# Optimization experiments

Measured on AMD Instinct MI355X. Metric: run time of the kernel, lower is better.

## Reference

```python
import jax, jax.numpy as jnp
import numpy as np

BATCH = 2048
VOCAB = 50257
TOPK = 512


def setup_inputs() -> dict:
    key = jax.random.key(0)
    k1, k2 = jax.random.split(key)
    features = jax.random.normal(k1, (BATCH, VOCAB), dtype=jnp.float32)
    labels = jax.random.randint(k2, (BATCH,), 0, VOCAB, dtype=jnp.int64 if jax.config.jax_enable_x64 else jnp.int32)
    return {"features": features, "labels": labels, "k": TOPK}


def reference(features, labels, k):
    # features: [B, V], labels: [B], k: python int (top-k count)
    # Original per-sample loop computes: -log(exp(feat_label) / sum(exp(topk(row))))
    # Vectorized: mean over batch of (log(sum(exp(topk_vals))) - feat_label).
    feat_label = jnp.take_along_axis(features, labels[:, None].astype(jnp.int32), axis=1)[:, 0]  # [B]
    topk_vals, _ = jax.lax.top_k(features, k)  # [B, k]
    lse = jnp.log(jnp.sum(jnp.exp(topk_vals), axis=-1))  # [B] (matches original non-stabilized math)
    return jnp.mean(lse - feat_label)
```

## Files before the change

### kernel.cpp

```cpp
#include <hip/hip_runtime.h>
#include <cstdint>
#include <cstddef>

#define BATCH 2048
#define VOCAB 50257
#define TOPK  512
#define CAND_MAX 4096
#define BLOCK 256

typedef float vfloat4 __attribute__((ext_vector_type(4)));

__device__ __forceinline__ unsigned fkey(float f) {
    unsigned u = __float_as_uint(f);
    return (u & 0x80000000u) ? ~u : (u | 0x80000000u);
}
__device__ __forceinline__ float unfkey(unsigned k) {
    unsigned u = (k & 0x80000000u) ? (k & 0x7FFFFFFFu) : ~k;
    return __uint_as_float(u);
}

__global__ __launch_bounds__(BLOCK) void topk_ce_kernel(
    const float* __restrict__ feats,
    const int*   __restrict__ labels,
    float*       __restrict__ out)
{
    __shared__ float    cand[CAND_MAX];
    __shared__ int      s_cnt;
    __shared__ unsigned s_hist[256];
    __shared__ unsigned s_sfx[256];
    __shared__ int      s_dig, s_above;
    __shared__ float    s_psum[BLOCK / 64];
    __shared__ float    s_pcnt[BLOCK / 64];

    const int row = blockIdx.x;
    const int tid = threadIdx.x;
    const float* rp = feats + (size_t)row * VOCAB;

    uintptr_t a = (uintptr_t)rp;
    int head = ((int)((16u - (a & 15u)) & 15u)) >> 2;
    if (head > VOCAB) head = VOCAB;
    const int nvec = (VOCAB - head) >> 2;
    const int tailstart = head + nvec * 4;
    const vfloat4* vp = (const vfloat4*)(rp + head);
    const int nfull = nvec / (BLOCK * 4);
    const int restart = nfull * BLOCK * 4;

    float thresh = 2.0f;
    float blo = 0.0f, bhi = 0.0f;
    bool  has_lo = false, has_hi = false;
    float step = 1.0f;
    int   n_cand = 0;

#define APPEND1(x) do { if ((x) > thresh) { int p_ = atomicAdd(&s_cnt, 1); \
                        if (p_ < CAND_MAX) cand[p_] = (x); } } while (0)
#define APPEND4(v) do { APPEND1((v).x); APPEND1((v).y); APPEND1((v).z); APPEND1((v).w); } while (0)

    for (int attempt = 0; attempt < 40; ++attempt) {
        if (tid == 0) s_cnt = 0;
        __syncthreads();

        for (int i = tid; i < head; i += BLOCK) {
            float v = rp[i];
            APPEND1(v);
        }
        for (int it = 0; it < nfull; ++it) {
            const int base = it * (BLOCK * 4) + tid;
            vfloat4 v0 = __builtin_nontemporal_load(&vp[base]);
            vfloat4 v1 = __builtin_nontemporal_load(&vp[base + BLOCK]);
            vfloat4 v2 = __builtin_nontemporal_load(&vp[base + 2 * BLOCK]);
            vfloat4 v3 = __builtin_nontemporal_load(&vp[base + 3 * BLOCK]);
            APPEND4(v0); APPEND4(v1); APPEND4(v2); APPEND4(v3);
        }
        for (int i = restart + tid; i < nvec; i += BLOCK) {
            vfloat4 v = __builtin_nontemporal_load(&vp[i]);
            APPEND4(v);
        }
        for (int i = tailstart + tid; i < VOCAB; i += BLOCK) {
            float v = rp[i];
            APPEND1(v);
        }
        __syncthreads();
        n_cand = s_cnt;
        if (n_cand >= TOPK && n_cand <= CAND_MAX) break;
        if (n_cand < TOPK) { bhi = thresh; has_hi = true; }
        else               { blo = thresh; has_lo = true; }
        if (has_lo && has_hi)      thresh = 0.5f * (blo + bhi);
        else if (has_lo)          { thresh = blo + step; step *= 2.0f; }
        else                      { thresh = bhi - step; step *= 2.0f; }
        __syncthreads();
    }

    const int m  = (n_cand < CAND_MAX) ? n_cand : CAND_MAX;
    const int kk = (TOPK < m) ? TOPK : m;
    if (m == 0) return;

    unsigned pref = 0, maskhi = 0;
    int remain = kk;
    const int m_pad = ((m + BLOCK - 1) / BLOCK) * BLOCK;

    for (int sh = 24; sh >= 0; sh -= 8) {
        s_hist[tid] = 0;
        __syncthreads();

        for (int i = tid; i < m_pad; i += BLOCK) {
            bool valid = (i < m);
            unsigned key = valid ? fkey(cand[i]) : 0u;
            bool match = valid && ((key & maskhi) == pref);
            unsigned dig = (key >> sh) & 255u;
            unsigned long long mm = __ballot(match);
            if (mm) {
                int leader = __ffsll((unsigned long long)mm) - 1;
                unsigned ldig = __shfl(dig, leader);
                unsigned long long same = __ballot(match && (dig == ldig));
                if (same == mm) {
                    if ((tid & 63) == leader)
                        atomicAdd(&s_hist[ldig], (unsigned)__popcll(mm));
                } else if (match) {
                    atomicAdd(&s_hist[dig], 1u);
                }
            }
        }
        __syncthreads();

        s_sfx[tid] = s_hist[tid];
        __syncthreads();
        for (int off = 1; off < 256; off <<= 1) {
            unsigned add = (tid + off < 256) ? s_sfx[tid + off] : 0u;
            __syncthreads();
            s_sfx[tid] += add;
            __syncthreads();
        }
        unsigned my  = s_sfx[tid];
        unsigned nxt = (tid < 255) ? s_sfx[tid + 1] : 0u;
        if ((int)my >= remain && (tid == 255 || (int)nxt < remain)) {
            s_dig = tid;
            s_above = (int)nxt;
        }
        __syncthreads();
        remain -= s_above;
        pref   |= ((unsigned)s_dig) << sh;
        maskhi |= (0xFFu << sh);
        __syncthreads();
    }

    const float tval = unfkey(pref);

    float psum = 0.0f, pcnt = 0.0f;
    for (int i = tid; i < m; i += BLOCK) {
        float v = cand[i];
        if (fkey(v) > pref) { psum += expf(v); pcnt += 1.0f; }
    }
    for (int off = 32; off > 0; off >>= 1) {
        psum += __shfl_down(psum, off);
        pcnt += __shfl_down(pcnt, off);
    }
    const int lane = tid & 63, wid = tid >> 6;
    if (lane == 0) { s_psum[wid] = psum; s_pcnt[wid] = pcnt; }
    __syncthreads();
    if (tid == 0) {
        float sum = 0.0f, cnt = 0.0f;
        for (int w = 0; w < BLOCK / 64; ++w) { sum += s_psum[w]; cnt += s_pcnt[w]; }
        sum += ((float)kk - cnt) * expf(tval);
        float fl = rp[labels[row]];
        float loss = logf(sum) - fl;
        atomicAdd(out, loss * (1.0f / (float)BATCH));
    }
}

extern "C" void kernel_launch(void* const* d_in, const int* in_sizes, int n_in,
                              void* d_out, int out_size, void* d_ws, size_t ws_size,
                              hipStream_t stream) {
    const float* feats  = (const float*)d_in[0];
    const int*   labels = (const int*)d_in[1];
    float* out = (float*)d_out;
    (void)in_sizes; (void)n_in; (void)out_size; (void)d_ws; (void)ws_size;

    (void)hipMemsetAsync(out, 0, sizeof(float), stream);
    topk_ce_kernel<<<BATCH, BLOCK, 0, stream>>>(feats, labels, out);
}
```

Measured before the change: 525.2 us.

## Replace shared atomic candidate append with per-thread LDS buckets and prefix compaction

```diff
diff --git a/kernel.cpp b/kernel.cpp
--- a/kernel.cpp
+++ b/kernel.cpp
@@ -5,8 +5,10 @@
 #define BATCH 2048
 #define VOCAB 50257
 #define TOPK  512
-#define CAND_MAX 4096
 #define BLOCK 256
+#define SLOTS 16
+#define STRIDE 17
+#define CAND_MAX (BLOCK * SLOTS)
 
 typedef float vfloat4 __attribute__((ext_vector_type(4)));
 
@@ -24,17 +26,17 @@
     const int*   __restrict__ labels,
     float*       __restrict__ out)
 {
-    __shared__ float    cand[CAND_MAX];
-    __shared__ int      s_cnt;
+    __shared__ float    buck[BLOCK * STRIDE];
+    __shared__ unsigned s_pfx[BLOCK];
     __shared__ unsigned s_hist[256];
-    __shared__ unsigned s_sfx[256];
-    __shared__ int      s_dig, s_above;
-    __shared__ float    s_psum[BLOCK / 64];
-    __shared__ float    s_pcnt[BLOCK / 64];
+    __shared__ int      s_dig, s_above, s_ovf;
+    __shared__ float    s_red0[BLOCK / 64];
+    __shared__ float    s_red1[BLOCK / 64];
 
     const int row = blockIdx.x;
     const int tid = threadIdx.x;
     const float* rp = feats + (size_t)row * VOCAB;
+    const int bbase = tid * STRIDE;
 
     uintptr_t a = (uintptr_t)rp;
     int head = ((int)((16u - (a & 15u)) & 15u)) >> 2;
@@ -49,50 +51,71 @@
     float blo = 0.0f, bhi = 0.0f;
     bool  has_lo = false, has_hi = false;
     float step = 1.0f;
-    int   n_cand = 0;
-
-#define APPEND1(x) do { if ((x) > thresh) { int p_ = atomicAdd(&s_cnt, 1); \
-                        if (p_ < CAND_MAX) cand[p_] = (x); } } while (0)
-#define APPEND4(v) do { APPEND1((v).x); APPEND1((v).y); APPEND1((v).z); APPEND1((v).w); } while (0)
+    int   cnt = 0;
+    unsigned total = 0;
+
+#define PUT1(x) do { float xv_ = (x); \
+                     int idx_ = (cnt < SLOTS) ? cnt : (SLOTS - 1); \
+                     buck[bbase + idx_] = xv_; \
+                     cnt += (xv_ > thresh) ? 1 : 0; } while (0)
+#define PUT4(v) do { PUT1((v).x); PUT1((v).y); PUT1((v).z); PUT1((v).w); } while (0)
 
     for (int attempt = 0; attempt < 40; ++attempt) {
-        if (tid == 0) s_cnt = 0;
-        __syncthreads();
-
-        for (int i = tid; i < head; i += BLOCK) {
-            float v = rp[i];
-            APPEND1(v);
-        }
+        if (tid == 0) s_ovf = 0;
+        cnt = 0;
+        __syncthreads();
+
+        for (int i = tid; i < head; i += BLOCK) PUT1(rp[i]);
         for (int it = 0; it < nfull; ++it) {
             const int base = it * (BLOCK * 4) + tid;
             vfloat4 v0 = __builtin_nontemporal_load(&vp[base]);
             vfloat4 v1 = __builtin_nontemporal_load(&vp[base + BLOCK]);
             vfloat4 v2 = __builtin_nontemporal_load(&vp[base + 2 * BLOCK]);
             vfloat4 v3 = __builtin_nontemporal_load(&vp[base + 3 * BLOCK]);
-            APPEND4(v0); APPEND4(v1); APPEND4(v2); APPEND4(v3);
+            PUT4(v0); PUT4(v1); PUT4(v2); PUT4(v3);
         }
         for (int i = restart + tid; i < nvec; i += BLOCK) {
             vfloat4 v = __builtin_nontemporal_load(&vp[i]);
-            APPEND4(v);
-        }
-        for (int i = tailstart + tid; i < VOCAB; i += BLOCK) {
-            float v = rp[i];
-            APPEND1(v);
-        }
-        __syncthreads();
-        n_cand = s_cnt;
-        if (n_cand >= TOPK && n_cand <= CAND_MAX) break;
-        if (n_cand < TOPK) { bhi = thresh; has_hi = true; }
-        else               { blo = thresh; has_lo = true; }
+            PUT4(v);
+        }
+        for (int i = tailstart + tid; i < VOCAB; i += BLOCK) PUT1(rp[i]);
+
+        if (cnt > SLOTS) { s_ovf = 1; cnt = SLOTS; }
+        s_pfx[tid] = (unsigned)cnt;
+        __syncthreads();
+
+        for (int off = 1; off < BLOCK; off <<= 1) {
+            unsigned add = (tid >= off) ? s_pfx[tid - off] : 0u;
+            __syncthreads();
+            s_pfx[tid] += add;
+            __syncthreads();
+        }
+        total = s_pfx[BLOCK - 1];
+        int ovf = s_ovf;
+        if (!ovf && total >= TOPK) break;
+        if (ovf) { blo = thresh; has_lo = true; }
+        else     { bhi = thresh; has_hi = true; }
         if (has_lo && has_hi)      thresh = 0.5f * (blo + bhi);
         else if (has_lo)          { thresh = blo + step; step *= 2.0f; }
         else                      { thresh = bhi - step; step *= 2.0f; }
         __syncthreads();
     }
 
-    const int m  = (n_cand < CAND_MAX) ? n_cand : CAND_MAX;
+    const int m  = (int)total;
     const int kk = (TOPK < m) ? TOPK : m;
     if (m == 0) return;
+
+    {
+        const unsigned pfx_excl = s_pfx[tid] - (unsigned)cnt;
+        float r[SLOTS];
+        #pragma unroll
+        for (int j = 0; j < SLOTS; ++j) r[j] = buck[bbase + j];
+        __syncthreads();
+        #pragma unroll
+        for (int j = 0; j < SLOTS; ++j)
+            if (j < cnt) buck[pfx_excl + j] = r[j];
+        __syncthreads();
+    }
 
     unsigned pref = 0, maskhi = 0;
     int remain = kk;
@@ -104,7 +127,7 @@
 
         for (int i = tid; i < m_pad; i += BLOCK) {
             bool valid = (i < m);
-            unsigned key = valid ? fkey(cand[i]) : 0u;
+            unsigned key = valid ? fkey(buck[i]) : 0u;
             bool match = valid && ((key & maskhi) == pref);
             unsigned dig = (key >> sh) & 255u;
             unsigned long long mm = __ballot(match);
@@ -122,16 +145,16 @@
         }
         __syncthreads();
 
-        s_sfx[tid] = s_hist[tid];
+        s_pfx[tid] = s_hist[tid];
         __syncthreads();
         for (int off = 1; off < 256; off <<= 1) {
-            unsigned add = (tid + off < 256) ? s_sfx[tid + off] : 0u;
-            __syncthreads();
-            s_sfx[tid] += add;
-            __syncthreads();
-        }
-        unsigned my  = s_sfx[tid];
-        unsigned nxt = (tid < 255) ? s_sfx[tid + 1] : 0u;
+            unsigned add = (tid + off < 256) ? s_pfx[tid + off] : 0u;
+            __syncthreads();
+            s_pfx[tid] += add;
+            __syncthreads();
+        }
+        unsigned my  = s_pfx[tid];
+        unsigned nxt = (tid < 255) ? s_pfx[tid + 1] : 0u;
         if ((int)my >= remain && (tid == 255 || (int)nxt < remain)) {
             s_dig = tid;
             s_above = (int)nxt;
@@ -147,7 +170,7 @@
 
     float psum = 0.0f, pcnt = 0.0f;
     for (int i = tid; i < m; i += BLOCK) {
-        float v = cand[i];
+        float v = buck[i];
         if (fkey(v) > pref) { psum += expf(v); pcnt += 1.0f; }
     }
     for (int off = 32; off > 0; off >>= 1) {
@@ -155,12 +178,12 @@
         pcnt += __shfl_down(pcnt, off);
     }
     const int lane = tid & 63, wid = tid >> 6;
-    if (lane == 0) { s_psum[wid] = psum; s_pcnt[wid] = pcnt; }
+    if (lane == 0) { s_red0[wid] = psum; s_red1[wid] = pcnt; }
     __syncthreads();
     if (tid == 0) {
-        float sum = 0.0f, cnt = 0.0f;
-        for (int w = 0; w < BLOCK / 64; ++w) { sum += s_psum[w]; cnt += s_pcnt[w]; }
-        sum += ((float)kk - cnt) * expf(tval);
+        float sum = 0.0f, c = 0.0f;
+        for (int w = 0; w < BLOCK / 64; ++w) { sum += s_red0[w]; c += s_red1[w]; }
+        sum += ((float)kk - c) * expf(tval);
         float fl = rp[labels[row]];
         float loss = logf(sum) - fl;
         atomicAdd(out, loss * (1.0f / (float)BATCH));
```

After: 542.8 us. 3.4% more time.
